# Performance work log

Measured on AMD Instinct MI355X. Metric: run time of the kernel, lower is better.

Reference implementation:

```python
import jax, jax.numpy as jnp
import numpy as np

# KroneckerLinear: W ~= sum_i (A_i kron B_i); efficient path computes, per token,
# Y = sum_i A_i @ X @ B_i^T with X = x.reshape(in1, in2), output flattened as (out1*out2).

IN1, IN2 = 64, 64      # in_factors (in1*in2 = in_features = 4096)
OUT1, OUT2 = 64, 64    # out_factors (out1*out2 = out_features = 4096)
NUM_SUM = 2
BATCH, SEQ = 4, 4096


def setup_inputs() -> dict:
    key = jax.random.key(0)
    kx, ka, kb, kbias = jax.random.split(key, 4)
    x = jax.random.normal(kx, (BATCH, SEQ, IN1 * IN2), dtype=jnp.float32)
    # kaiming-uniform-like scale for small factors
    bound_a = 1.0 / np.sqrt(IN1)
    bound_b = 1.0 / np.sqrt(IN2)
    A = jax.random.uniform(ka, (NUM_SUM, OUT1, IN1), dtype=jnp.float32, minval=-bound_a, maxval=bound_a)
    B = jax.random.uniform(kb, (NUM_SUM, OUT2, IN2), dtype=jnp.float32, minval=-bound_b, maxval=bound_b)
    bound = 1.0 / np.sqrt(IN1 * IN2)
    bias = jax.random.uniform(kbias, (OUT1 * OUT2,), dtype=jnp.float32, minval=-bound, maxval=bound)
    return {"x": x, "A": A, "B": B, "bias": bias}


def reference(x, A, B, bias):
    Bsz, T, _ = x.shape
    X = x.reshape(Bsz, T, IN1, IN2)  # (b, t, i, j)
    # y[b,t,o,p] = sum_s sum_ij A[s,o,i] * X[b,t,i,j] * B[s,p,j]  -> (out1, out2)
    y = jnp.einsum("btij,soi,spj->btop", X, A, B)
    return y.reshape(Bsz, T, OUT1 * OUT2) + bias
```

## Files before the change

### kernel.cpp

```cpp
#include <hip/hip_runtime.h>
#include <hip/hip_bf16.h>

typedef float  f32x4  __attribute__((ext_vector_type(4)));
typedef short  bf16x8 __attribute__((ext_vector_type(8)));

#define NT      16384
#define NBLOCK  512
#define TPS     (NT / NBLOCK)

__device__ __forceinline__ short f2bf(float x) {
  return (short)__builtin_bit_cast(unsigned short, __float2bfloat16(x));
}
__device__ __forceinline__ unsigned packbf2(float a, float b) {
  return (unsigned)(unsigned short)f2bf(a) | ((unsigned)(unsigned short)f2bf(b) << 16);
}

__device__ __forceinline__ void gload16(const float* gp, float* lp) {
  __builtin_amdgcn_global_load_lds((const __attribute__((address_space(1))) void*)gp,
                                   (__attribute__((address_space(3))) void*)lp,
                                   16, 0, 0);
}
__device__ __forceinline__ unsigned ldsaddr(const void* p) {
  return (unsigned)(uintptr_t)(const __attribute__((address_space(3))) void*)p;
}

__device__ __forceinline__ void stageQW(float* XB, const float* gbase, int w, int lane) {
#pragma unroll
  for (int qq = 0; qq < 4; ++qq) {
    const int q = w * 4 + qq;
    const int i = q * 4 + (lane >> 4);
    const float* gp = gbase + i * 64 + (((lane & 15) ^ (i & 7)) << 2);
    gload16(gp, XB + q * 256);
  }
}

__global__ __launch_bounds__(256, 2)
void kron_kernel(const float* __restrict__ x,
                 const float* __restrict__ A,
                 const float* __restrict__ Bm,
                 const float* __restrict__ bias,
                 float* __restrict__ out) {
  __shared__ float  xb[2][4096];
  __shared__ bf16x8 AT[1024];
  __shared__ bf16x8 BT[1024];
  __shared__ unsigned long long Ul[2048];

  const int tid  = threadIdx.x;
  const int lane = tid & 63;
  const int w    = tid >> 6;
  const int g    = lane >> 4;
  const int l15  = lane & 15;
  const int blk  = blockIdx.x;

#pragma unroll
  for (int t = 0; t < 4; ++t) {
    const int idx = w * 4 + t;
    const int s = idx >> 3, ot = (idx & 7) >> 1, c = idx & 1;
    const int o = ot * 16 + l15;
    bf16x8 v;
#pragma unroll
    for (int e = 0; e < 8; ++e) {
      const int i = c * 32 + 4 * g + (e & 3) + 16 * (e >> 2);
      v[e] = f2bf(A[s * 4096 + o * 64 + i]);
    }
    AT[idx * 64 + lane] = v;
  }
#pragma unroll
  for (int t = 0; t < 4; ++t) {
    const int idx = w * 4 + t;
    const int s = idx >> 3, pt = (idx & 7) >> 1, jc = idx & 1;
    const int p = pt * 16 + l15;
    bf16x8 v;
#pragma unroll
    for (int e = 0; e < 8; ++e)
      v[e] = f2bf(Bm[s * 4096 + p * 64 + (jc * 32 + 8 * g + e)]);
    BT[idx * 64 + lane] = v;
  }

  f32x4 bv[4];
#pragma unroll
  for (int ot = 0; ot < 4; ++ot)
    bv[ot] = *(const f32x4*)(bias + (ot * 16 + l15) * 64 + w * 16 + 4 * g);

  __syncthreads();

  stageQW(&xb[0][0], x + ((size_t)blk << 12), w, lane);
  stageQW(&xb[1][0], x + ((size_t)(blk + NBLOCK) << 12), w, lane);
  asm volatile("s_waitcnt vmcnt(4)" ::: "memory");
  __builtin_amdgcn_s_barrier();

  const unsigned wsw = (unsigned)(2 * ((l15 >> 2) & 1));

  for (int k = 0; k < TPS; ++k) {
    const unsigned ba   = ldsaddr(&xb[k & 1][0]);
    const unsigned base = ba + (unsigned)(w * 16 + l15) * 256u;
    const unsigned m    = (unsigned)(l15 & 7);
    f32x4 r0[2], r1[2];
#pragma unroll
    for (int jc = 0; jc < 2; ++jc) {
      const unsigned c0 = (unsigned)(8 * jc + 2 * g);
      asm volatile("ds_read_b128 %0, %1" : "=v"(r0[jc]) : "v"(base + ((c0 ^ m) << 4)) : "memory");
      asm volatile("ds_read_b128 %0, %1" : "=v"(r1[jc]) : "v"(base + (((c0 + 1u) ^ m) << 4)) : "memory");
    }
    asm volatile("s_waitcnt lgkmcnt(0)" ::: "memory");
    __builtin_amdgcn_sched_barrier(0);

    bf16x8 xf[2];
#pragma unroll
    for (int jc = 0; jc < 2; ++jc) {
      bf16x8 t;
      t[0]=f2bf(r0[jc][0]); t[1]=f2bf(r0[jc][1]); t[2]=f2bf(r0[jc][2]); t[3]=f2bf(r0[jc][3]);
      t[4]=f2bf(r1[jc][0]); t[5]=f2bf(r1[jc][1]); t[6]=f2bf(r1[jc][2]); t[7]=f2bf(r1[jc][3]);
      xf[jc] = t;
    }

#pragma unroll
    for (int s = 0; s < 2; ++s) {
#pragma unroll
      for (int pt = 0; pt < 4; ++pt) {
        f32x4 a1 = (f32x4){0.f, 0.f, 0.f, 0.f};
#pragma unroll
        for (int jc = 0; jc < 2; ++jc)
          a1 = __builtin_amdgcn_mfma_f32_16x16x32_bf16(
              xf[jc], BT[(s * 8 + pt * 2 + jc) * 64 + lane], a1, 0, 0, 0);
        const unsigned lo = packbf2(a1[0], a1[1]);
        const unsigned hi = packbf2(a1[2], a1[3]);
        Ul[((((s * 4 + pt) * 4 + g) * 16 + l15) << 2) + ((unsigned)w ^ wsw)] =
            ((unsigned long long)hi << 32) | lo;
      }
    }

    asm volatile("s_waitcnt lgkmcnt(0)" ::: "memory");
    __builtin_amdgcn_sched_barrier(0);
    __builtin_amdgcn_s_barrier();

    if (k + 2 < TPS)
      stageQW(&xb[k & 1][0], x + ((size_t)(blk + (k + 2) * NBLOCK) << 12), w, lane);

    f32x4 acc[4];
#pragma unroll
    for (int ot = 0; ot < 4; ++ot) acc[ot] = bv[ot];
#pragma unroll
    for (int s = 0; s < 2; ++s) {
      bf16x8 uf[2];
#pragma unroll
      for (int c = 0; c < 2; ++c) {
        const unsigned q2 = (unsigned)((l15 >> 2) & 1);
        uf[c] = *reinterpret_cast<const bf16x8*>(
            &Ul[((((s * 4 + w) * 4 + g) * 16 + l15) << 2) + 2u * ((unsigned)c ^ q2)]);
      }
#pragma unroll
      for (int ot = 0; ot < 4; ++ot)
#pragma unroll
        for (int c = 0; c < 2; ++c)
          acc[ot] = __builtin_amdgcn_mfma_f32_16x16x32_bf16(
              uf[c], AT[(s * 8 + ot * 2 + c) * 64 + lane], acc[ot], 0, 0, 0);
    }

    float* ob = out + ((size_t)(blk + k * NBLOCK) << 12);
#pragma unroll
    for (int ot = 0; ot < 4; ++ot)
      *(f32x4*)(ob + (ot * 16 + l15) * 64 + w * 16 + 4 * g) = acc[ot];

    asm volatile("s_waitcnt vmcnt(8) lgkmcnt(0)" ::: "memory");
    __builtin_amdgcn_sched_barrier(0);
    __builtin_amdgcn_s_barrier();
  }
}

extern "C" void kernel_launch(void* const* d_in, const int* in_sizes, int n_in,
                              void* d_out, int out_size, void* d_ws, size_t ws_size,
                              hipStream_t stream) {
  const float* x    = (const float*)d_in[0];
  const float* A    = (const float*)d_in[1];
  const float* B    = (const float*)d_in[2];
  const float* bias = (const float*)d_in[3];
  float* out        = (float*)d_out;
  kron_kernel<<<dim3(NBLOCK), dim3(256), 0, stream>>>(x, A, B, bias, out);
}
```

Measured before the change: 105.3 us.

## Warp-specialize into producer and consumer waves with 4-stage LDS ring

Splits each 512-thread block into four producer waves that issue global-to-LDS loads of x and four consumer waves that run both MFMA stages and store outputs. The x buffer grows from two to four stages, with prefetch distance 3, and the grid halves to 256 blocks with one block per CU. The goal is to overlap global loads with compute more fully. In exchange, occupancy drops to one block, the producer waves hold no compute work, and the grid of 256 blocks is matched to the CU count.

Result: faster. 100.5 us (-4.6%).

```diff
diff --git a/kernel.cpp b/kernel.cpp
--- a/kernel.cpp
+++ b/kernel.cpp
@@ -5,7 +5,7 @@
 typedef short  bf16x8 __attribute__((ext_vector_type(8)));
 
 #define NT      16384
-#define NBLOCK  512
+#define NBLOCK  256
 #define TPS     (NT / NBLOCK)
 
 __device__ __forceinline__ short f2bf(float x) {
@@ -24,23 +24,23 @@
   return (unsigned)(uintptr_t)(const __attribute__((address_space(3))) void*)p;
 }
 
-__device__ __forceinline__ void stageQW(float* XB, const float* gbase, int w, int lane) {
+__device__ __forceinline__ void stageQW(float* XB, const float* gbase, int j, int lane) {
 #pragma unroll
   for (int qq = 0; qq < 4; ++qq) {
-    const int q = w * 4 + qq;
+    const int q = j * 4 + qq;
     const int i = q * 4 + (lane >> 4);
     const float* gp = gbase + i * 64 + (((lane & 15) ^ (i & 7)) << 2);
     gload16(gp, XB + q * 256);
   }
 }
 
-__global__ __launch_bounds__(256, 2)
+__global__ __launch_bounds__(512, 1)
 void kron_kernel(const float* __restrict__ x,
                  const float* __restrict__ A,
                  const float* __restrict__ Bm,
                  const float* __restrict__ bias,
                  float* __restrict__ out) {
-  __shared__ float  xb[2][4096];
+  __shared__ float  xb[4][4096];
   __shared__ bf16x8 AT[1024];
   __shared__ bf16x8 BT[1024];
   __shared__ unsigned long long Ul[2048];
@@ -48,122 +48,133 @@
   const int tid  = threadIdx.x;
   const int lane = tid & 63;
   const int w    = tid >> 6;
+  const int j    = w & 3;
   const int g    = lane >> 4;
   const int l15  = lane & 15;
   const int blk  = blockIdx.x;
-
-#pragma unroll
-  for (int t = 0; t < 4; ++t) {
-    const int idx = w * 4 + t;
-    const int s = idx >> 3, ot = (idx & 7) >> 1, c = idx & 1;
-    const int o = ot * 16 + l15;
-    bf16x8 v;
-#pragma unroll
-    for (int e = 0; e < 8; ++e) {
-      const int i = c * 32 + 4 * g + (e & 3) + 16 * (e >> 2);
-      v[e] = f2bf(A[s * 4096 + o * 64 + i]);
-    }
-    AT[idx * 64 + lane] = v;
-  }
-#pragma unroll
-  for (int t = 0; t < 4; ++t) {
-    const int idx = w * 4 + t;
-    const int s = idx >> 3, pt = (idx & 7) >> 1, jc = idx & 1;
-    const int p = pt * 16 + l15;
-    bf16x8 v;
-#pragma unroll
-    for (int e = 0; e < 8; ++e)
-      v[e] = f2bf(Bm[s * 4096 + p * 64 + (jc * 32 + 8 * g + e)]);
-    BT[idx * 64 + lane] = v;
-  }
+  const bool consumer = (w < 4);
 
   f32x4 bv[4];
+  if (consumer) {
 #pragma unroll
-  for (int ot = 0; ot < 4; ++ot)
-    bv[ot] = *(const f32x4*)(bias + (ot * 16 + l15) * 64 + w * 16 + 4 * g);
-
+    for (int t = 0; t < 4; ++t) {
+      const int idx = j * 4 + t;
+      const int s = idx >> 3, ot = (idx & 7) >> 1, c = idx & 1;
+      const int o = ot * 16 + l15;
+      bf16x8 v;
+#pragma unroll
+      for (int e = 0; e < 8; ++e) {
+        const int i = c * 32 + 4 * g + (e & 3) + 16 * (e >> 2);
+        v[e] = f2bf(A[s * 4096 + o * 64 + i]);
+      }
+      AT[idx * 64 + lane] = v;
+    }
+#pragma unroll
+    for (int t = 0; t < 4; ++t) {
+      const int idx = j * 4 + t;
+      const int s = idx >> 3, pt = (idx & 7) >> 1, jc = idx & 1;
+      const int p = pt * 16 + l15;
+      bf16x8 v;
+#pragma unroll
+      for (int e = 0; e < 8; ++e)
+        v[e] = f2bf(Bm[s * 4096 + p * 64 + (jc * 32 + 8 * g + e)]);
+      BT[idx * 64 + lane] = v;
+    }
+#pragma unroll
+    for (int ot = 0; ot < 4; ++ot)
+      bv[ot] = *(const f32x4*)(bias + (ot * 16 + l15) * 64 + j * 16 + 4 * g);
+  }
   __syncthreads();
 
-  stageQW(&xb[0][0], x + ((size_t)blk << 12), w, lane);
-  stageQW(&xb[1][0], x + ((size_t)(blk + NBLOCK) << 12), w, lane);
-  asm volatile("s_waitcnt vmcnt(4)" ::: "memory");
+  if (!consumer) {
+    stageQW(&xb[0][0], x + ((size_t)blk << 12),                j, lane);
+    stageQW(&xb[1][0], x + ((size_t)(blk + NBLOCK) << 12),     j, lane);
+    stageQW(&xb[2][0], x + ((size_t)(blk + 2 * NBLOCK) << 12), j, lane);
+    asm volatile("s_waitcnt vmcnt(8)" ::: "memory");
+  }
   __builtin_amdgcn_s_barrier();
 
   const unsigned wsw = (unsigned)(2 * ((l15 >> 2) & 1));
 
   for (int k = 0; k < TPS; ++k) {
-    const unsigned ba   = ldsaddr(&xb[k & 1][0]);
-    const unsigned base = ba + (unsigned)(w * 16 + l15) * 256u;
-    const unsigned m    = (unsigned)(l15 & 7);
-    f32x4 r0[2], r1[2];
+    if (consumer) {
+      const unsigned ba   = ldsaddr(&xb[k & 3][0]);
+      const unsigned base = ba + (unsigned)(j * 16 + l15) * 256u;
+      const unsigned m    = (unsigned)(l15 & 7);
+      f32x4 r0[2], r1[2];
 #pragma unroll
-    for (int jc = 0; jc < 2; ++jc) {
-      const unsigned c0 = (unsigned)(8 * jc + 2 * g);
-      asm volatile("ds_read_b128 %0, %1" : "=v"(r0[jc]) : "v"(base + ((c0 ^ m) << 4)) : "memory");
-      asm volatile("ds_read_b128 %0, %1" : "=v"(r1[jc]) : "v"(base + (((c0 + 1u) ^ m) << 4)) : "memory");
-    }
-    asm volatile("s_waitcnt lgkmcnt(0)" ::: "memory");
-    __builtin_amdgcn_sched_barrier(0);
+      for (int jc = 0; jc < 2; ++jc) {
+        const unsigned c0 = (unsigned)(8 * jc + 2 * g);
+        asm volatile("ds_read_b128 %0, %1" : "=v"(r0[jc]) : "v"(base + ((c0 ^ m) << 4)) : "memory");
+        asm volatile("ds_read_b128 %0, %1" : "=v"(r1[jc]) : "v"(base + (((c0 + 1u) ^ m) << 4)) : "memory");
+      }
+      asm volatile("s_waitcnt lgkmcnt(0)" ::: "memory");
+      __builtin_amdgcn_sched_barrier(0);
 
-    bf16x8 xf[2];
+      bf16x8 xf[2];
 #pragma unroll
-    for (int jc = 0; jc < 2; ++jc) {
-      bf16x8 t;
-      t[0]=f2bf(r0[jc][0]); t[1]=f2bf(r0[jc][1]); t[2]=f2bf(r0[jc][2]); t[3]=f2bf(r0[jc][3]);
-      t[4]=f2bf(r1[jc][0]); t[5]=f2bf(r1[jc][1]); t[6]=f2bf(r1[jc][2]); t[7]=f2bf(r1[jc][3]);
-      xf[jc] = t;
+      for (int jc = 0; jc < 2; ++jc) {
+        bf16x8 t;
+        t[0]=f2bf(r0[jc][0]); t[1]=f2bf(r0[jc][1]); t[2]=f2bf(r0[jc][2]); t[3]=f2bf(r0[jc][3]);
+        t[4]=f2bf(r1[jc][0]); t[5]=f2bf(r1[jc][1]); t[6]=f2bf(r1[jc][2]); t[7]=f2bf(r1[jc][3]);
+        xf[jc] = t;
+      }
+
+#pragma unroll
+      for (int s = 0; s < 2; ++s) {
+#pragma unroll
+        for (int pt = 0; pt < 4; ++pt) {
+          f32x4 a1 = (f32x4){0.f, 0.f, 0.f, 0.f};
+#pragma unroll
+          for (int jc = 0; jc < 2; ++jc)
+            a1 = __builtin_amdgcn_mfma_f32_16x16x32_bf16(
+                xf[jc], BT[(s * 8 + pt * 2 + jc) * 64 + lane], a1, 0, 0, 0);
+          const unsigned lo = packbf2(a1[0], a1[1]);
+          const unsigned hi = packbf2(a1[2], a1[3]);
+          Ul[((((s * 4 + pt) * 4 + g) * 16 + l15) << 2) + ((unsigned)j ^ wsw)] =
+              ((unsigned long long)hi << 32) | lo;
+        }
+      }
+      asm volatile("s_waitcnt lgkmcnt(0)" ::: "memory");
+      __builtin_amdgcn_sched_barrier(0);
+    } else {
+      if (k + 3 < TPS)
+        stageQW(&xb[(k + 3) & 3][0],
+                x + ((size_t)(blk + (k + 3) * NBLOCK) << 12), j, lane);
     }
 
+    __builtin_amdgcn_s_barrier();
+
+    if (consumer) {
+      f32x4 acc[4];
 #pragma unroll
-    for (int s = 0; s < 2; ++s) {
+      for (int ot = 0; ot < 4; ++ot) acc[ot] = bv[ot];
 #pragma unroll
-      for (int pt = 0; pt < 4; ++pt) {
-        f32x4 a1 = (f32x4){0.f, 0.f, 0.f, 0.f};
+      for (int s = 0; s < 2; ++s) {
+        bf16x8 uf[2];
 #pragma unroll
-        for (int jc = 0; jc < 2; ++jc)
-          a1 = __builtin_amdgcn_mfma_f32_16x16x32_bf16(
-              xf[jc], BT[(s * 8 + pt * 2 + jc) * 64 + lane], a1, 0, 0, 0);
-        const unsigned lo = packbf2(a1[0], a1[1]);
-        const unsigned hi = packbf2(a1[2], a1[3]);
-        Ul[((((s * 4 + pt) * 4 + g) * 16 + l15) << 2) + ((unsigned)w ^ wsw)] =
-            ((unsigned long long)hi << 32) | lo;
+        for (int c = 0; c < 2; ++c) {
+          const unsigned q2 = (unsigned)((l15 >> 2) & 1);
+          uf[c] = *reinterpret_cast<const bf16x8*>(
+              &Ul[((((s * 4 + j) * 4 + g) * 16 + l15) << 2) + 2u * ((unsigned)c ^ q2)]);
+        }
+#pragma unroll
+        for (int ot = 0; ot < 4; ++ot)
+#pragma unroll
+          for (int c = 0; c < 2; ++c)
+            acc[ot] = __builtin_amdgcn_mfma_f32_16x16x32_bf16(
+                uf[c], AT[(s * 8 + ot * 2 + c) * 64 + lane], acc[ot], 0, 0, 0);
       }
+      float* ob = out + ((size_t)(blk + k * NBLOCK) << 12);
+#pragma unroll
+      for (int ot = 0; ot < 4; ++ot)
+        *(f32x4*)(ob + (ot * 16 + l15) * 64 + j * 16 + 4 * g) = acc[ot];
+    } else {
+      if (k < TPS - 3)       asm volatile("s_waitcnt vmcnt(8)" ::: "memory");
+      else if (k == TPS - 3) asm volatile("s_waitcnt vmcnt(4)" ::: "memory");
+      else                   asm volatile("s_waitcnt vmcnt(0)" ::: "memory");
     }
 
-    asm volatile("s_waitcnt lgkmcnt(0)" ::: "memory");
-    __builtin_amdgcn_sched_barrier(0);
-    __builtin_amdgcn_s_barrier();
-
-    if (k + 2 < TPS)
-      stageQW(&xb[k & 1][0], x + ((size_t)(blk + (k + 2) * NBLOCK) << 12), w, lane);
-
-    f32x4 acc[4];
-#pragma unroll
-    for (int ot = 0; ot < 4; ++ot) acc[ot] = bv[ot];
-#pragma unroll
-    for (int s = 0; s < 2; ++s) {
-      bf16x8 uf[2];
-#pragma unroll
-      for (int c = 0; c < 2; ++c) {
-        const unsigned q2 = (unsigned)((l15 >> 2) & 1);
-        uf[c] = *reinterpret_cast<const bf16x8*>(
-            &Ul[((((s * 4 + w) * 4 + g) * 16 + l15) << 2) + 2u * ((unsigned)c ^ q2)]);
-      }
-#pragma unroll
-      for (int ot = 0; ot < 4; ++ot)
-#pragma unroll
-        for (int c = 0; c < 2; ++c)
-          acc[ot] = __builtin_amdgcn_mfma_f32_16x16x32_bf16(
-              uf[c], AT[(s * 8 + ot * 2 + c) * 64 + lane], acc[ot], 0, 0, 0);
-    }
-
-    float* ob = out + ((size_t)(blk + k * NBLOCK) << 12);
-#pragma unroll
-    for (int ot = 0; ot < 4; ++ot)
-      *(f32x4*)(ob + (ot * 16 + l15) * 64 + w * 16 + 4 * g) = acc[ot];
-
-    asm volatile("s_waitcnt vmcnt(8) lgkmcnt(0)" ::: "memory");
-    __builtin_amdgcn_sched_barrier(0);
     __builtin_amdgcn_s_barrier();
   }
 }
@@ -176,5 +187,5 @@
   const float* B    = (const float*)d_in[2];
   const float* bias = (const float*)d_in[3];
   float* out        = (float*)d_out;
-  kron_kernel<<<dim3(NBLOCK), dim3(256), 0, stream>>>(x, A, B, bias, out);
+  kron_kernel<<<dim3(NBLOCK), dim3(512), 0, stream>>>(x, A, B, bias, out);
 }
```
